# Kernel optimization log

Measured on AMD Instinct MI355X. Metric: run time of the kernel, lower is better.

## Reference

```python
import jax, jax.numpy as jnp
import numpy as np

N = 100000       # nodes
E = 640000       # edges
G = 2048         # graphs in batch
IN_C, HID, NCLS = 3, 128, 4


def setup_inputs() -> dict:
    key = jax.random.key(0)
    ks = jax.random.split(key, 16)
    x = jax.random.normal(ks[0], (N, IN_C), dtype=jnp.float32)
    edge_index = jax.random.randint(ks[1], (2, E), 0, N, dtype=jnp.int64)
    batch = jnp.sort(jax.random.randint(ks[2], (N,), 0, G, dtype=jnp.int64))
    def glorot(k, shape):
        lim = np.sqrt(6.0 / (shape[0] + shape[1])).astype(np.float32)
        return jax.random.uniform(k, shape, jnp.float32, -lim, lim)
    return {
        "x": x, "edge_index": edge_index, "batch": batch,
        "W1": glorot(ks[3], (IN_C, HID)), "b1": jnp.zeros((HID,), jnp.float32),
        "W2": glorot(ks[4], (HID, HID)),  "b2": jnp.zeros((HID,), jnp.float32),
        "W3": glorot(ks[5], (HID, HID)),  "b3": jnp.zeros((HID,), jnp.float32),
        "W4": glorot(ks[6], (HID, HID)),  "b4": jnp.zeros((HID,), jnp.float32),
        "Wfc": glorot(ks[7], (HID, NCLS)), "bfc": jnp.zeros((NCLS,), jnp.float32),
    }


def _gcn_norm(edge_index):
    # Add self loops, then symmetric normalization D^{-1/2} (A+I) D^{-1/2}.
    loop = jnp.arange(N, dtype=edge_index.dtype)
    row = jnp.concatenate([edge_index[0], loop])  # source
    col = jnp.concatenate([edge_index[1], loop])  # target (aggregation side)
    deg = jax.ops.segment_sum(jnp.ones_like(col, dtype=jnp.float32), col,
                              num_segments=N)
    dinv = jnp.where(deg > 0, jax.lax.rsqrt(deg), 0.0)
    norm = dinv[row] * dinv[col]  # [E+N]
    return row, col, norm


def _gcn_layer(x, W, b, row, col, norm):
    h = x @ W                                 # [N, out]
    msg = h[row] * norm[:, None]              # gather + scale, [E+N, out]
    out = jax.ops.segment_sum(msg, col, num_segments=N)
    return out + b


def reference(x, edge_index, batch, W1, b1, W2, b2, W3, b3, W4, b4, Wfc, bfc):
    row, col, norm = _gcn_norm(edge_index)
    h = jax.nn.relu(_gcn_layer(x, W1, b1, row, col, norm))
    h = jax.nn.relu(_gcn_layer(h, W2, b2, row, col, norm))
    h = jax.nn.relu(_gcn_layer(h, W3, b3, row, col, norm))
    h = jax.nn.relu(_gcn_layer(h, W4, b4, row, col, norm))
    # global mean pool over graphs
    sums = jax.ops.segment_sum(h, batch, num_segments=G)           # [G, HID]
    cnt = jax.ops.segment_sum(jnp.ones((N,), jnp.float32), batch,
                              num_segments=G)
    pooled = sums / jnp.maximum(cnt, 1.0)[:, None]
    return pooled @ Wfc + bfc                                      # [G, NCLS]
```

## Files before the change

kernel.cpp:

```cpp
#include <hip/hip_runtime.h>
#include <hip/hip_bf16.h>

#define N_NODES  100000
#define N_EDGES  640000
#define N_GRAPHS 2048
#define HID      128
#define NB_SCAN  391
#define TILE     64

typedef _Float16 half_t;
typedef __attribute__((ext_vector_type(4))) _Float16 half4;
typedef __attribute__((ext_vector_type(8))) _Float16 half8;
typedef __attribute__((ext_vector_type(4))) float floatx4;

__global__ void k_prep(const int* __restrict__ col, int* __restrict__ deg,
                       const float* __restrict__ x, float4* __restrict__ xp,
                       const float* __restrict__ W2, const float* __restrict__ W3,
                       const float* __restrict__ W4, half_t* __restrict__ Wt) {
    int idx = blockIdx.x * 256 + threadIdx.x;
    if (idx < N_EDGES) atomicAdd(&deg[col[idx]], 1);
    if (idx < N_NODES) xp[idx] = make_float4(x[idx * 3 + 0], x[idx * 3 + 1], x[idx * 3 + 2], 0.f);
    if (idx < 3 * 128 * 128) {
        int l = idx >> 14;
        int e = idx & 16383;
        int cin = e >> 7, cout = e & 127;
        const float* W = (l == 0) ? W2 : ((l == 1) ? W3 : W4);
        Wt[l * 16384 + cout * 128 + cin] = (half_t)W[cin * 128 + cout];
    }
}

__global__ void k_scan1(const int* __restrict__ deg, int* __restrict__ row_ptr,
                        int* __restrict__ bsum, float* __restrict__ dinv) {
    __shared__ int s[256];
    int tid = threadIdx.x;
    int i = blockIdx.x * 256 + tid;
    int d = (i < N_NODES) ? deg[i] : 0;
    if (i < N_NODES) dinv[i] = rsqrtf((float)(d + 1));
    s[tid] = d;
    __syncthreads();
    for (int off = 1; off < 256; off <<= 1) {
        int v = (tid >= off) ? s[tid - off] : 0;
        __syncthreads();
        s[tid] += v;
        __syncthreads();
    }
    if (i < N_NODES) row_ptr[i] = s[tid] - d;
    if (tid == 255) bsum[blockIdx.x] = s[255];
}

__global__ void k_scan2(int* __restrict__ bsum) {
    __shared__ int s[512];
    int tid = threadIdx.x;
    int v = (tid < NB_SCAN) ? bsum[tid] : 0;
    s[tid] = v;
    __syncthreads();
    for (int off = 1; off < 512; off <<= 1) {
        int u = (tid >= off) ? s[tid - off] : 0;
        __syncthreads();
        s[tid] += u;
        __syncthreads();
    }
    if (tid < NB_SCAN) bsum[tid] = s[tid] - v;
}

__global__ void k_scan3(int* __restrict__ row_ptr, const int* __restrict__ bsum) {
    int i = blockIdx.x * 256 + threadIdx.x;
    if (i < N_NODES) row_ptr[i] += bsum[blockIdx.x];
    if (i == N_NODES) row_ptr[N_NODES] = N_EDGES;
}

__global__ void k_scatter(const int* __restrict__ row, const int* __restrict__ col,
                          const int* __restrict__ row_ptr, int* __restrict__ cursor,
                          const float* __restrict__ dinv, int2* __restrict__ epair) {
    int e = blockIdx.x * blockDim.x + threadIdx.x;
    if (e >= N_EDGES) return;
    int c = col[e];
    int r = row[e];
    int p = row_ptr[c] + atomicAdd(&cursor[c], 1);
    epair[p] = make_int2(r, __float_as_int(dinv[r] * dinv[c]));
}

__global__ __launch_bounds__(256) void k_aggx_fc1(const float4* __restrict__ xp,
                                                  const int* __restrict__ row_ptr,
                                                  const int2* __restrict__ epair,
                                                  const float* __restrict__ dinv,
                                                  const float* __restrict__ W1,
                                                  const float* __restrict__ b1,
                                                  half_t* __restrict__ h) {
    __shared__ float sax[256][3];
    int t = threadIdx.x;
    int nb = blockIdx.x * 256;
    int i = nb + t;
    if (i < N_NODES) {
        float di = dinv[i];
        float sw = di * di;
        float4 xv = xp[i];
        float a0 = sw * xv.x, a1 = sw * xv.y, a2 = sw * xv.z;
        int s = row_ptr[i], e = row_ptr[i + 1];
        int k = s;
        for (; k + 4 <= e; k += 4) {
            int2 pr[4];
#pragma unroll
            for (int r = 0; r < 4; r++) pr[r] = epair[k + r];
            float4 bx[4];
#pragma unroll
            for (int r = 0; r < 4; r++) bx[r] = xp[pr[r].x];
#pragma unroll
            for (int r = 0; r < 4; r++) {
                float w = __int_as_float(pr[r].y);
                a0 += w * bx[r].x;
                a1 += w * bx[r].y;
                a2 += w * bx[r].z;
            }
        }
        for (; k < e; k++) {
            int2 pr = epair[k];
            float w = __int_as_float(pr.y);
            float4 bx = xp[pr.x];
            a0 += w * bx.x;
            a1 += w * bx.y;
            a2 += w * bx.z;
        }
        sax[t][0] = a0; sax[t][1] = a1; sax[t][2] = a2;
    }
    __syncthreads();
    int cq = t & 31, g8 = t >> 5;
    const float4* W14 = (const float4*)W1;
    float4 w0 = W14[cq], w1 = W14[32 + cq], w2 = W14[64 + cq];
    float4 bb = ((const float4*)b1)[cq];
    for (int pass = 0; pass < 32; pass++) {
        int local = pass * 8 + g8;
        int node = nb + local;
        if (node >= N_NODES) break;
        float x0 = sax[local][0], x1 = sax[local][1], x2 = sax[local][2];
        half4 o;
        o.x = (half_t)fmaxf(bb.x + x0 * w0.x + x1 * w1.x + x2 * w2.x, 0.f);
        o.y = (half_t)fmaxf(bb.y + x0 * w0.y + x1 * w1.y + x2 * w2.y, 0.f);
        o.z = (half_t)fmaxf(bb.z + x0 * w0.z + x1 * w1.z + x2 * w2.z, 0.f);
        o.w = (half_t)fmaxf(bb.w + x0 * w0.w + x1 * w1.w + x2 * w2.w, 0.f);
        ((half4*)h)[(size_t)node * 32 + cq] = o;
    }
}

__global__ __launch_bounds__(256, 8) void k_agg(const half_t* __restrict__ h_in,
                                                const int* __restrict__ row_ptr,
                                                const int2* __restrict__ epair,
                                                const float* __restrict__ dinv,
                                                half_t* __restrict__ g) {
    int tid = threadIdx.x;
    int lane16 = tid & 15;
    int i = blockIdx.x * 16 + (tid >> 4);
    if (i >= N_NODES) return;
    const half8* h8 = (const half8*)h_in;

    float di = dinv[i];
    float sw = di * di;
    half8 v = h8[(size_t)i * 16 + lane16];
    float acc[8];
#pragma unroll
    for (int c = 0; c < 8; c++) acc[c] = sw * (float)v[c];

    int s = row_ptr[i], e = row_ptr[i + 1];
    if (s < e) {
        int em1 = e - 1;
        int2 p0 = epair[s];
        int k1 = min(s + 1, em1);
        int2 p1 = epair[k1];
        float w0 = __int_as_float(p0.y);
        float w1 = (s + 1 < e) ? __int_as_float(p1.y) : 0.f;
        half8 u0 = h8[(size_t)p0.x * 16 + lane16];
        half8 u1 = h8[(size_t)p1.x * 16 + lane16];
        for (int k = s; k < e; k += 2) {
            int k2 = min(k + 2, em1);
            int k3 = min(k + 3, em1);
            int2 p2 = epair[k2];
            int2 p3 = epair[k3];
            float w2 = (k + 2 < e) ? __int_as_float(p2.y) : 0.f;
            float w3 = (k + 3 < e) ? __int_as_float(p3.y) : 0.f;
            half8 n0 = h8[(size_t)p2.x * 16 + lane16];
            half8 n1 = h8[(size_t)p3.x * 16 + lane16];
#pragma unroll
            for (int c = 0; c < 8; c++) acc[c] += w0 * (float)u0[c] + w1 * (float)u1[c];
            u0 = n0; u1 = n1; w0 = w2; w1 = w3;
        }
    }
    half8 av;
#pragma unroll
    for (int c = 0; c < 8; c++) av[c] = (half_t)acc[c];
    ((half8*)g)[(size_t)i * 16 + lane16] = av;
}

__global__ __launch_bounds__(256) void k_mm(const half_t* __restrict__ g,
                                            const half_t* __restrict__ Wt,
                                            const float* __restrict__ b,
                                            half_t* __restrict__ h_out) {
    __shared__ half_t gs[TILE][128];
    int tid = threadIdx.x;
    int n0 = blockIdx.x * TILE;

    const int4* gsrc = (const int4*)(g + (size_t)n0 * 128);
    int4* gdst = (int4*)&gs[0][0];
    for (int idx = tid; idx < TILE * 16; idx += 256) {
        int node = n0 + (idx >> 4);
        int4 vv;
        if (node < N_NODES) vv = gsrc[idx];
        else { vv.x = vv.y = vv.z = vv.w = 0; }
        gdst[idx] = vv;
    }
    __syncthreads();

    int wv = tid >> 6;
    int ln = tid & 15;
    int q  = (tid >> 4) & 3;
    floatx4 C[8];
#pragma unroll
    for (int t = 0; t < 8; t++) {
        float bn = b[t * 16 + ln];
        C[t].x = bn; C[t].y = bn; C[t].z = bn; C[t].w = bn;
    }
#pragma unroll
    for (int kq = 0; kq < 4; kq++) {
        half8 a = *(const half8*)(&gs[wv * 16 + ln][kq * 32 + q * 8]);
#pragma unroll
        for (int t = 0; t < 8; t++) {
            half8 bf = *(const half8*)(Wt + (size_t)(t * 16 + ln) * 128 + kq * 32 + q * 8);
            C[t] = __builtin_amdgcn_mfma_f32_16x16x32_f16(a, bf, C[t], 0, 0, 0);
        }
    }

    __syncthreads();
#pragma unroll
    for (int t = 0; t < 8; t++) {
#pragma unroll
        for (int reg = 0; reg < 4; reg++) {
            float dv = (reg == 0) ? C[t].x : (reg == 1) ? C[t].y : (reg == 2) ? C[t].z : C[t].w;
            gs[wv * 16 + q * 4 + reg][t * 16 + ln] = (half_t)fmaxf(dv, 0.f);
        }
    }
    __syncthreads();
    int r0 = tid >> 2;
    int c0 = (tid & 3) * 4;
    int node = n0 + r0;
    if (node < N_NODES) {
        int4* dst = (int4*)(h_out + (size_t)node * 128);
        const int4* srcp = (const int4*)(&gs[r0][0]);
#pragma unroll
        for (int kk = 0; kk < 4; kk++) dst[c0 + kk] = srcp[c0 + kk];
    }
}

__global__ __launch_bounds__(128) void k_pool_final(const half_t* __restrict__ h,
                                                    const int* __restrict__ batch,
                                                    const float* __restrict__ Wfc,
                                                    const float* __restrict__ bfc,
                                                    float* __restrict__ out) {
    __shared__ float sred[8][128];
    __shared__ float red[128][4];
    __shared__ int sb_s, eb_s;
    int g = blockIdx.x, t = threadIdx.x;
    if (t == 0) {
        int lo = 0, hi = N_NODES;
        while (lo < hi) { int mid = (lo + hi) >> 1; if (batch[mid] < g) lo = mid + 1; else hi = mid; }
        sb_s = lo;
        hi = N_NODES;
        while (lo < hi) { int mid = (lo + hi) >> 1; if (batch[mid] < g + 1) lo = mid + 1; else hi = mid; }
        eb_s = lo;
    }
    __syncthreads();
    int sb = sb_s, eb = eb_s;
    int lane16 = t & 15, slot = t >> 4;
    const half8* h8 = (const half8*)h;
    float acc[8];
#pragma unroll
    for (int c = 0; c < 8; c++) acc[c] = 0.f;
    for (int n = sb + slot; n < eb; n += 8) {
        half8 v = h8[(size_t)n * 16 + lane16];
#pragma unroll
        for (int c = 0; c < 8; c++) acc[c] += (float)v[c];
    }
#pragma unroll
    for (int c = 0; c < 8; c++) sred[slot][lane16 * 8 + c] = acc[c];
    __syncthreads();
    float pv = 0.f;
#pragma unroll
    for (int s2 = 0; s2 < 8; s2++) pv += sred[s2][t];
    float inv = 1.0f / fmaxf((float)(eb - sb), 1.0f);
    float v = pv * inv;
    float4 w = ((const float4*)Wfc)[t];
    red[t][0] = v * w.x; red[t][1] = v * w.y; red[t][2] = v * w.z; red[t][3] = v * w.w;
    __syncthreads();
    for (int s = 64; s > 0; s >>= 1) {
        if (t < s) {
            red[t][0] += red[t + s][0];
            red[t][1] += red[t + s][1];
            red[t][2] += red[t + s][2];
            red[t][3] += red[t + s][3];
        }
        __syncthreads();
    }
    if (t < 4) out[g * 4 + t] = red[0][t] + bfc[t];
}

extern "C" void kernel_launch(void* const* d_in, const int* in_sizes, int n_in,
                              void* d_out, int out_size, void* d_ws, size_t ws_size,
                              hipStream_t stream) {
    const float* x     = (const float*)d_in[0];
    const int*   ei    = (const int*)d_in[1];
    const int*   row   = ei;
    const int*   col   = ei + N_EDGES;
    const int*   batch = (const int*)d_in[2];
    const float* W1 = (const float*)d_in[3];
    const float* b1 = (const float*)d_in[4];
    const float* W2 = (const float*)d_in[5];
    const float* b2 = (const float*)d_in[6];
    const float* W3 = (const float*)d_in[7];
    const float* b3 = (const float*)d_in[8];
    const float* W4 = (const float*)d_in[9];
    const float* b4 = (const float*)d_in[10];
    const float* Wfc = (const float*)d_in[11];
    const float* bfc = (const float*)d_in[12];
    float* out = (float*)d_out;

    char* ws = (char*)d_ws;
    size_t off = 0;
    auto take = [&](size_t bytes) -> char* {
        char* p = ws + off;
        off = (off + bytes + 255) & ~(size_t)255;
        return p;
    };
    int*    deg     = (int*)take(N_NODES * 4);
    int*    cursor  = (int*)take(N_NODES * 4);
    size_t  zspan   = (size_t)((char*)cursor + N_NODES * 4 - (char*)deg);
    int*    row_ptr = (int*)take((N_NODES + 1) * 4);
    int*    bsum    = (int*)take(512 * 4);
    float*  dinv    = (float*)take(N_NODES * 4);
    float4* xp      = (float4*)take((size_t)N_NODES * 16);
    int2*   epair   = (int2*)take((size_t)N_EDGES * 8);
    half_t* wt16    = (half_t*)take((size_t)3 * 128 * 128 * 2);
    half_t* bufA    = (half_t*)take((size_t)N_NODES * 128 * 2);
    half_t* bufB    = (half_t*)take((size_t)N_NODES * 128 * 2);

    hipMemsetAsync(deg, 0, zspan, stream);

    k_prep<<<(N_EDGES + 255) / 256, 256, 0, stream>>>(col, deg, x, xp, W2, W3, W4, wt16);
    k_scan1<<<NB_SCAN, 256, 0, stream>>>(deg, row_ptr, bsum, dinv);
    k_scan2<<<1, 512, 0, stream>>>(bsum);
    k_scan3<<<NB_SCAN, 256, 0, stream>>>(row_ptr, bsum);
    k_scatter<<<(N_EDGES + 255) / 256, 256, 0, stream>>>(row, col, row_ptr, cursor,
                                                         dinv, epair);
    k_aggx_fc1<<<NB_SCAN, 256, 0, stream>>>(xp, row_ptr, epair, dinv, W1, b1, bufA);

    const int NBA = (N_NODES + 15) / 16;
    const int NBM = (N_NODES + TILE - 1) / TILE;
    k_agg<<<NBA, 256, 0, stream>>>(bufA, row_ptr, epair, dinv, bufB);
    k_mm<<<NBM, 256, 0, stream>>>(bufB, wt16, b2, bufA);
    k_agg<<<NBA, 256, 0, stream>>>(bufA, row_ptr, epair, dinv, bufB);
    k_mm<<<NBM, 256, 0, stream>>>(bufB, wt16 + 16384, b3, bufA);
    k_agg<<<NBA, 256, 0, stream>>>(bufA, row_ptr, epair, dinv, bufB);
    k_mm<<<NBM, 256, 0, stream>>>(bufB, wt16 + 32768, b4, bufA);

    k_pool_final<<<N_GRAPHS, 128, 0, stream>>>(bufA, batch, Wfc, bfc, out);
}
```

Before: 385.7 us.

## Fuse neighbor aggregation with dense layer matmul into one kernel per layer

Merges the gather-aggregate kernel and the MFMA matmul kernel so each block aggregates 64 nodes straight into shared memory and then multiplies by the weight matrix. This drops the write and re-read of the intermediate aggregated buffer and halves the kernel launches per layer. The shared tile is padded to a 136-element stride to reduce bank conflicts. In exchange, each block now serializes four aggregation passes before the matmul, with fewer blocks and a lower occupancy hint, so latency hiding for the irregular gathers may suffer.

```diff
diff --git a/kernel.cpp b/kernel.cpp
--- a/kernel.cpp
+++ b/kernel.cpp
@@ -7,6 +7,7 @@
 #define HID      128
 #define NB_SCAN  391
 #define TILE     64
+#define LDW      136
 
 typedef _Float16 half_t;
 typedef __attribute__((ext_vector_type(4))) _Float16 half4;
@@ -142,70 +143,62 @@
     }
 }
 
-__global__ __launch_bounds__(256, 8) void k_agg(const half_t* __restrict__ h_in,
-                                                const int* __restrict__ row_ptr,
-                                                const int2* __restrict__ epair,
-                                                const float* __restrict__ dinv,
-                                                half_t* __restrict__ g) {
-    int tid = threadIdx.x;
-    int lane16 = tid & 15;
-    int i = blockIdx.x * 16 + (tid >> 4);
-    if (i >= N_NODES) return;
-    const half8* h8 = (const half8*)h_in;
-
-    float di = dinv[i];
-    float sw = di * di;
-    half8 v = h8[(size_t)i * 16 + lane16];
-    float acc[8];
-#pragma unroll
-    for (int c = 0; c < 8; c++) acc[c] = sw * (float)v[c];
-
-    int s = row_ptr[i], e = row_ptr[i + 1];
-    if (s < e) {
-        int em1 = e - 1;
-        int2 p0 = epair[s];
-        int k1 = min(s + 1, em1);
-        int2 p1 = epair[k1];
-        float w0 = __int_as_float(p0.y);
-        float w1 = (s + 1 < e) ? __int_as_float(p1.y) : 0.f;
-        half8 u0 = h8[(size_t)p0.x * 16 + lane16];
-        half8 u1 = h8[(size_t)p1.x * 16 + lane16];
-        for (int k = s; k < e; k += 2) {
-            int k2 = min(k + 2, em1);
-            int k3 = min(k + 3, em1);
-            int2 p2 = epair[k2];
-            int2 p3 = epair[k3];
-            float w2 = (k + 2 < e) ? __int_as_float(p2.y) : 0.f;
-            float w3 = (k + 3 < e) ? __int_as_float(p3.y) : 0.f;
-            half8 n0 = h8[(size_t)p2.x * 16 + lane16];
-            half8 n1 = h8[(size_t)p3.x * 16 + lane16];
-#pragma unroll
-            for (int c = 0; c < 8; c++) acc[c] += w0 * (float)u0[c] + w1 * (float)u1[c];
-            u0 = n0; u1 = n1; w0 = w2; w1 = w3;
-        }
-    }
-    half8 av;
-#pragma unroll
-    for (int c = 0; c < 8; c++) av[c] = (half_t)acc[c];
-    ((half8*)g)[(size_t)i * 16 + lane16] = av;
-}
-
-__global__ __launch_bounds__(256) void k_mm(const half_t* __restrict__ g,
-                                            const half_t* __restrict__ Wt,
-                                            const float* __restrict__ b,
-                                            half_t* __restrict__ h_out) {
-    __shared__ half_t gs[TILE][128];
+__global__ __launch_bounds__(256, 4) void k_agg_mm(const half_t* __restrict__ h_in,
+                                                   const int* __restrict__ row_ptr,
+                                                   const int2* __restrict__ epair,
+                                                   const float* __restrict__ dinv,
+                                                   const half_t* __restrict__ Wt,
+                                                   const float* __restrict__ b,
+                                                   half_t* __restrict__ h_out) {
+    __shared__ __align__(16) half_t gs[TILE][LDW];
     int tid = threadIdx.x;
     int n0 = blockIdx.x * TILE;
-
-    const int4* gsrc = (const int4*)(g + (size_t)n0 * 128);
-    int4* gdst = (int4*)&gs[0][0];
-    for (int idx = tid; idx < TILE * 16; idx += 256) {
-        int node = n0 + (idx >> 4);
-        int4 vv;
-        if (node < N_NODES) vv = gsrc[idx];
-        else { vv.x = vv.y = vv.z = vv.w = 0; }
-        gdst[idx] = vv;
+    int lane16 = tid & 15;
+    int gidx = tid >> 4;
+    const half8* h8 = (const half8*)h_in;
+
+    for (int p = 0; p < 4; p++) {
+        int local = p * 16 + gidx;
+        int i = n0 + local;
+        half8 av;
+        if (i < N_NODES) {
+            float di = dinv[i];
+            float sw = di * di;
+            half8 v = h8[(size_t)i * 16 + lane16];
+            float acc[8];
+#pragma unroll
+            for (int c = 0; c < 8; c++) acc[c] = sw * (float)v[c];
+            int s = row_ptr[i], e = row_ptr[i + 1];
+            if (s < e) {
+                int em1 = e - 1;
+                int2 p0 = epair[s];
+                int k1 = min(s + 1, em1);
+                int2 p1 = epair[k1];
+                float w0 = __int_as_float(p0.y);
+                float w1 = (s + 1 < e) ? __int_as_float(p1.y) : 0.f;
+                half8 u0 = h8[(size_t)p0.x * 16 + lane16];
+                half8 u1 = h8[(size_t)p1.x * 16 + lane16];
+                for (int k = s; k < e; k += 2) {
+                    int k2 = min(k + 2, em1);
+                    int k3 = min(k + 3, em1);
+                    int2 p2 = epair[k2];
+                    int2 p3 = epair[k3];
+                    float w2 = (k + 2 < e) ? __int_as_float(p2.y) : 0.f;
+                    float w3 = (k + 3 < e) ? __int_as_float(p3.y) : 0.f;
+                    half8 m0 = h8[(size_t)p2.x * 16 + lane16];
+                    half8 m1 = h8[(size_t)p3.x * 16 + lane16];
+#pragma unroll
+                    for (int c = 0; c < 8; c++) acc[c] += w0 * (float)u0[c] + w1 * (float)u1[c];
+                    u0 = m0; u1 = m1; w0 = w2; w1 = w3;
+                }
+            }
+#pragma unroll
+            for (int c = 0; c < 8; c++) av[c] = (half_t)acc[c];
+        } else {
+#pragma unroll
+            for (int c = 0; c < 8; c++) av[c] = (half_t)0.f;
+        }
+        *(half8*)(&gs[local][lane16 * 8]) = av;
     }
     __syncthreads();
 
@@ -350,14 +343,10 @@
                                                          dinv, epair);
     k_aggx_fc1<<<NB_SCAN, 256, 0, stream>>>(xp, row_ptr, epair, dinv, W1, b1, bufA);
 
-    const int NBA = (N_NODES + 15) / 16;
-    const int NBM = (N_NODES + TILE - 1) / TILE;
-    k_agg<<<NBA, 256, 0, stream>>>(bufA, row_ptr, epair, dinv, bufB);
-    k_mm<<<NBM, 256, 0, stream>>>(bufB, wt16, b2, bufA);
-    k_agg<<<NBA, 256, 0, stream>>>(bufA, row_ptr, epair, dinv, bufB);
-    k_mm<<<NBM, 256, 0, stream>>>(bufB, wt16 + 16384, b3, bufA);
-    k_agg<<<NBA, 256, 0, stream>>>(bufA, row_ptr, epair, dinv, bufB);
-    k_mm<<<NBM, 256, 0, stream>>>(bufB, wt16 + 32768, b4, bufA);
-
-    k_pool_final<<<N_GRAPHS, 128, 0, stream>>>(bufA, batch, Wfc, bfc, out);
-}
+    const int NBF = (N_NODES + TILE - 1) / TILE;
+    k_agg_mm<<<NBF, 256, 0, stream>>>(bufA, row_ptr, epair, dinv, wt16,         b2, bufB);
+    k_agg_mm<<<NBF, 256, 0, stream>>>(bufB, row_ptr, epair, dinv, wt16 + 16384, b3, bufA);
+    k_agg_mm<<<NBF, 256, 0, stream>>>(bufA, row_ptr, epair, dinv, wt16 + 32768, b4, bufB);
+
+    k_pool_final<<<N_GRAPHS, 128, 0, stream>>>(bufB, batch, Wfc, bfc, out);
+}
```

Measured after the change: 369.1 us. -4.3%, faster.
